# Optimization experiments

Hardware: AMD Instinct MI355X
Metric: run time of the kernel (lower is better)

Reference implementation:

```python
import jax, jax.numpy as jnp
import numpy as np

N_PIECES = 4
N_ACTIONS = 4
H = W = 4


def _conv3x3(x, w, b):
    # x: [B,C,H,W], w: [O,C,3,3] (torch OIHW), padding=1
    y = jax.lax.conv_general_dilated(x, w, window_strides=(1, 1), padding=((1, 1), (1, 1)),
                                     dimension_numbers=('NCHW', 'OIHW', 'NCHW'))
    return y + b[None, :, None, None]


def _conv1x1(x, w, b):
    # 1x1 conv as einsum; w: [O,C,1,1]
    return jnp.einsum('bchw,oc->bohw', x, w[:, :, 0, 0]) + b[None, :, None, None]


def setup_inputs() -> dict:
    key = jax.random.key(0)
    ks = jax.random.split(key, 20)
    B = 131072
    ob = jax.random.randint(ks[0], (B, H, W), 0, N_PIECES)
    ac = jax.random.randint(ks[1], (B,), 0, N_ACTIONS)

    def rnd(k, shape, fan_in):
        bound = 1.0 / np.sqrt(fan_in)
        return jax.random.uniform(k, shape, jnp.float32, -bound, bound)

    p = {}
    p['w_start1'] = rnd(ks[2], (32, N_PIECES + N_ACTIONS, 3, 3), 8 * 9)
    p['b_start1'] = rnd(ks[3], (32,), 8 * 9)
    p['w_start2'] = rnd(ks[4], (16, 32, 1, 1), 32)
    p['b_start2'] = rnd(ks[5], (16,), 32)
    p['w_ob1'] = rnd(ks[6], (16, 16, 1, 1), 16)
    p['b_ob1'] = rnd(ks[7], (16,), 16)
    p['w_ob2'] = rnd(ks[8], (N_PIECES * 2, 16 + N_PIECES, 1, 1), 20)
    p['b_ob2'] = rnd(ks[9], (N_PIECES * 2,), 20)
    p['w_reward'] = rnd(ks[10], (8, 16, 1, 1), 16)
    p['b_reward'] = rnd(ks[11], (8,), 16)
    p['fc_reward_w'] = rnd(ks[12], (4, 8 * H * W), 8 * H * W)
    p['fc_reward_b'] = rnd(ks[13], (4,), 8 * H * W)
    p['w_go'] = rnd(ks[14], (8, 16, 1, 1), 16)
    p['b_go'] = rnd(ks[15], (8,), 16)
    p['fc_go_w'] = rnd(ks[16], (4, 8 * H * W), 8 * H * W)
    p['fc_go_b'] = rnd(ks[17], (4,), 8 * H * W)
    return {'ob': ob, 'ac': ac, **p}


def reference(ob, ac, w_start1, b_start1, w_start2, b_start2, w_ob1, b_ob1, w_ob2, b_ob2,
              w_reward, b_reward, fc_reward_w, fc_reward_b, w_go, b_go, fc_go_w, fc_go_b):
    B = ob.shape[0]
    # one-hot encode board and action
    ob_oh = (ob[:, None, :, :] == jnp.arange(N_PIECES)[None, :, None, None]).astype(jnp.float32)  # [B,4,4,4]
    ac_oh = (ac[:, None] == jnp.arange(N_ACTIONS)[None, :]).astype(jnp.float32)  # [B,4]
    ac_map = jnp.broadcast_to(ac_oh[:, :, None, None], (B, N_ACTIONS, H, W))
    x = jnp.concatenate([ob_oh, ac_map], axis=1)  # [B,8,4,4]

    x = jax.nn.relu(_conv3x3(x, w_start1, b_start1))
    x = jax.nn.relu(_conv1x1(x, w_start2, b_start2))  # [B,16,4,4]

    # next-ob head
    nol = jax.nn.relu(_conv1x1(x, w_ob1, b_ob1))
    nol = jnp.concatenate([nol, ob_oh], axis=1)  # [B,20,4,4]
    nol = _conv1x1(nol, w_ob2, b_ob2)  # [B,8,4,4]
    nol = jnp.transpose(nol, (0, 2, 3, 1))  # [B,4,4,8]
    next_ob_loc = nol[..., :N_PIECES]
    next_ob_scale = nol[..., N_PIECES:]

    # reward head
    r = jax.nn.relu(_conv1x1(x, w_reward, b_reward)).reshape(B, -1)
    r = r @ fc_reward_w.T + fc_reward_b
    reward_loc, reward_scale = r[:, :2], r[:, 2:]

    # game-over head
    g = jax.nn.relu(_conv1x1(x, w_go, b_go)).reshape(B, -1)
    g = g @ fc_go_w.T + fc_go_b
    go_loc, go_scale = g[:, :2], g[:, 2:]

    return (next_ob_loc, next_ob_scale, reward_loc, reward_scale, go_loc, go_scale)
```

## Files before the change

kernel.cpp:

```cpp
#include <hip/hip_runtime.h>
#include <hip/hip_bf16.h>

typedef unsigned short u16;
typedef unsigned int u32;
typedef unsigned long long u64;

typedef _Float16 vh8 __attribute__((ext_vector_type(8)));
typedef _Float16 hv2 __attribute__((ext_vector_type(2)));
typedef __attribute__((ext_vector_type(16))) float vf16;

#define A1_OFF   0
#define A2_OFF   1280
#define A3_OFF   2048
#define A4_OFF   2560
#define FH_OFF   3072
#define FB_OFF   4096
#define FLAG_OFF 4104
#define T_OFF    4160

__device__ __forceinline__ float bf2f(u16 h){ union{u32 u; float f;} v; v.u=((u32)h)<<16; return v.f; }
__device__ __forceinline__ u16 f2h(float f){ _Float16 h=(_Float16)f; return __builtin_bit_cast(u16,h); }
__device__ __forceinline__ float ldw(const void* p,int i,bool bf){ return bf? bf2f(((const u16*)p)[i]) : ((const float*)p)[i]; }

__device__ __forceinline__ bool detect_bf16(const void* w1){
  const u16* p=(const u16*)w1; bool ok=true;
  for(int k=0;k<64;++k){ float v=bf2f(p[k]); ok &= (fabsf(v)<=0.125f); }
  return ok;
}

__device__ __constant__ int PI[32] = {0,1,2,3,8,9,10,11,4,5,6,7,12,13,14,15,
                                      16,17,18,19,24,25,26,27,20,21,22,23,28,29,30,31};

__global__ __launch_bounds__(256) void dw_prep(
    const void* w1, const void* b1, const void* w2, const void* b2,
    const void* wo1, const void* bo1, const void* wo2, const void* bo2,
    const void* wr, const void* br, const void* fcr, const void* fbr,
    const void* wg, const void* bg, const void* fcg, const void* fbg,
    u32* wsu){
  const int tid = threadIdx.x;
  const bool bf = detect_bf16(w1);
  float* wsf = (float*)wsu;

  for (int t=tid; t<768; t+=256){
    int kb=t>>8, l=(t>>2)&63, r=t&3, hi=l>>5, row=l&31;
    u32 w=0;
    for (int u=0;u<2;++u){
      int m=2*r+u, tt=m>>2, q=m&3, s=2*kb+tt;
      int pos = 2*s+hi;
      float v=0.f;
      if (s<5 && pos<=8) v = ldw(w1, row*72 + q*9 + pos, bf);
      w |= ((u32)f2h(v)) << (16*u);
    }
    wsu[A1_OFF+t]=w;
  }
  for (int t=tid; t<2048; t+=256){
    int a=t>>9, hi=(t>>8)&1, rq=(t>>6)&3, c16=(t>>2)&15, rl=t&3;
    int row = rl + 8*rq + 4*hi;
    int ci=c16>>2, cj=c16&3;
    float s0 = ldw(b1, row, bf);
    for (int dy=0; dy<3; ++dy)
      for (int dx=0; dx<3; ++dx){
        int ni=ci+dy-1, nj=cj+dx-1;
        if (ni>=0&&ni<4&&nj>=0&&nj<4)
          s0 += ldw(w1, row*72 + (4+a)*9 + dy*3+dx, bf);
      }
    wsf[T_OFF+t] = s0;
  }
  for (int t=tid; t<768; t+=256){
    int kb=t>>8, l=(t>>2)&63, r=t&3, hi=l>>5, row=l&31;
    int K0=kb*16+hi*8+2*r; u32 w=0;
    for (int s=0;s<2;++s){
      int K=K0+s; float v=0.f;
      if (K<32){ if(row<16) v=ldw(w2, row*32+PI[K], bf); }
      else if (K==32 && row<16) v=ldw(b2, row, bf);
      w |= ((u32)f2h(v)) << (16*s);
    }
    wsu[A2_OFF+t]=w;
  }
  for (int t=tid; t<512; t+=256){
    int kb=t>>8, l=(t>>2)&63, r=t&3, hi=l>>5, row=l&31;
    int K0=kb*16+hi*8+2*r; u32 w=0;
    for (int s=0;s<2;++s){
      int K=K0+s; float v=0.f;
      if (K<16){
        int c=PI[K];
        v = (row<16)? ldw(wo1,row*16+c,bf) : (row<24)? ldw(wr,(row-16)*16+c,bf) : ldw(wg,(row-24)*16+c,bf);
      } else if (K==16){
        v = (row<16)? ldw(bo1,row,bf) : (row<24)? ldw(br,row-16,bf) : ldw(bg,row-24,bf);
      }
      w |= ((u32)f2h(v)) << (16*s);
    }
    wsu[A3_OFF+t]=w;
  }
  for (int t=tid; t<512; t+=256){
    int kb=t>>8, l=(t>>2)&63, r=t&3, hi=l>>5, row=l&31;
    int K0=kb*16+hi*8+2*r; u32 w=0;
    for (int s=0;s<2;++s){
      int K=K0+s; float v=0.f;
      if (row<8){
        if (K<16)              v=ldw(wo2, row*20+PI[K], bf);
        else if (K==16)        v=ldw(bo2, row, bf);
        else if (K>=17&&K<=20) v=ldw(wo2, row*20+16+(K-17), bf);
      }
      w |= ((u32)f2h(v)) << (16*s);
    }
    wsu[A4_OFF+t]=w;
  }
  for (int t=tid; t<512; t+=256){
    int head=t>>8, r=t&255, hi=r>>7, c16=(r>>3)&15, k=(r>>1)&3, j=r&1;
    const void* f = head ? fcg : fcr;
    float v0 = ldw(f, k*128+(4*hi+2*j)*16+c16, bf);
    float v1 = ldw(f, k*128+(4*hi+2*j+1)*16+c16, bf);
    wsu[FH_OFF+t] = (u32)f2h(v0) | ((u32)f2h(v1)<<16);
  }
  for (int t=tid; t<8; t+=256) wsf[FB_OFF+t] = ldw(t<4?fbr:fbg, t&3, bf);
  if (tid==0) wsu[FLAG_OFF] = bf ? 1u : 0u;
}

__host__ __device__ constexpr u32 nbpgen(int c, int hi){
  u32 v=0;
  for (int s=0;s<5;++s){
    int pos=2*s+hi; u32 f=32;
    if (pos<=8){
      int ni=c/4+pos/3-1, nj=c%4+pos%3-1;
      if (ni>=0&&ni<4&&nj>=0&&nj<4) f=(u32)((ni*4+nj)<<1);
    }
    v |= f << (6*s);
  }
  return v;
}
__device__ __constant__ u32 NBP[32] = {
  nbpgen(0,0),nbpgen(1,0),nbpgen(2,0),nbpgen(3,0),nbpgen(4,0),nbpgen(5,0),nbpgen(6,0),nbpgen(7,0),
  nbpgen(8,0),nbpgen(9,0),nbpgen(10,0),nbpgen(11,0),nbpgen(12,0),nbpgen(13,0),nbpgen(14,0),nbpgen(15,0),
  nbpgen(0,1),nbpgen(1,1),nbpgen(2,1),nbpgen(3,1),nbpgen(4,1),nbpgen(5,1),nbpgen(6,1),nbpgen(7,1),
  nbpgen(8,1),nbpgen(9,1),nbpgen(10,1),nbpgen(11,1),nbpgen(12,1),nbpgen(13,1),nbpgen(14,1),nbpgen(15,1)};

__device__ __forceinline__ vf16 mfma(int4 a, int4 b, vf16 c){
  union{int4 i; vh8 v;} ua, ub; ua.i=a; ub.i=b;
  return __builtin_amdgcn_mfma_f32_32x32x16_f16(ua.v, ub.v, c, 0, 0, 0);
}
__device__ __forceinline__ u32 pkh(float a, float b){
#if __has_builtin(__builtin_amdgcn_cvt_pkrtz)
  auto h = __builtin_amdgcn_cvt_pkrtz(a, b);
  return __builtin_bit_cast(u32, h);
#else
  return (u32)f2h(a) | ((u32)f2h(b)<<16);
#endif
}
__device__ __forceinline__ u32 pkmax0(u32 x){
  u32 d; asm("v_pk_max_f16 %0, %1, 0" : "=v"(d) : "v"(x)); return d;
}
__device__ __forceinline__ float dot2(u32 w, u32 x, float c){
#if __has_builtin(__builtin_amdgcn_fdot2)
  return __builtin_amdgcn_fdot2(__builtin_bit_cast(hv2,w), __builtin_bit_cast(hv2,x), c, false);
#else
  hv2 a=__builtin_bit_cast(hv2,w), b=__builtin_bit_cast(hv2,x);
  return c + (float)a[0]*(float)b[0] + (float)a[1]*(float)b[1];
#endif
}
__device__ __forceinline__ u32 pkbf(float a, float b){
  u16 lo=__builtin_bit_cast(u16,__float2bfloat16(a));
  u16 hi=__builtin_bit_cast(u16,__float2bfloat16(b));
  return (u32)lo | ((u32)hi<<16);
}
template<int CTRL> __device__ __forceinline__ float dppadd(float x){
  int y=__builtin_amdgcn_update_dpp(0,__builtin_bit_cast(int,x),CTRL,0xF,0xF,false);
  return x+__builtin_bit_cast(float,y);
}
template<int CTRL> __device__ __forceinline__ u32 dppor(u32 x){
  u32 y=(u32)__builtin_amdgcn_update_dpp(0,(int)x,CTRL,0xF,0xF,false);
  return x|y;
}
template<int CTRL> __device__ __forceinline__ float dppmov(float x){
  int y=__builtin_amdgcn_update_dpp(0,__builtin_bit_cast(int,x),CTRL,0xF,0xF,false);
  return __builtin_bit_cast(float,y);
}

__global__ __launch_bounds__(512) void dw_main(
    const int* __restrict__ ob, const int* __restrict__ ac,
    const u32* __restrict__ g, void* __restrict__ outp, int B){
  __shared__ int4 sW4[576];
  __shared__ float4 sT4[512];
  const int4* gA = (const int4*)g;
  const float4* gT = (const float4*)g;

  const int tid  = threadIdx.x;
  if (tid < 512) sW4[tid] = gA[320+tid];
  if (tid < 64)  sW4[512+tid] = gA[320+512+tid];
  sT4[tid] = gT[(T_OFF>>2)+tid];
  __syncthreads();

  const int lane = tid & 63;
  const int hi   = lane >> 5;
  const int col  = lane & 31;
  const int c16  = col & 15;
  const int elem = col >> 4;
  const int wid  = tid >> 6;
  const bool obf = g[FLAG_OFF] != 0u;
  const float* gS = (const float*)g;

  const u32 nbp = NBP[(hi<<4)|c16];
  const int4 bconst = make_int4(hi?0:0x3C00, 0, 0, 0);
  const vf16 zero = {0.f,0.f,0.f,0.f,0.f,0.f,0.f,0.f,0.f,0.f,0.f,0.f,0.f,0.f,0.f,0.f};
  const int xaddr = (lane^32)<<2;

  const int e = (int)(blockIdx.x<<4) + (wid<<1) + elem;
  const bool act = (e < B);
  const int eL = act ? e : 0;

  u32 pkv = ((u32)ob[(size_t)eL*16 + c16]) << (c16<<1);
  pkv = dppor<0x121>(pkv);
  pkv = dppor<0x122>(pkv);
  pkv = dppor<0x124>(pkv);
  pkv = dppor<0x128>(pkv);
  const int a = ac[eL];

  int4 breg[3];
#pragma unroll
  for (int kb=0;kb<3;++kb){
    u32 w[4];
#pragma unroll
    for (int t=0;t<2;++t){
      const int s = kb*2+t;
      u32 w0=0, w1=0;
      if (s < 5){
        u32 v = (nbp >> (6*s)) & 63u;
        u32 np = (pkv >> (v & 31u)) & 3u;
        u32 src = (v < 32u) ? 0x3C00u : 0u;
        u64 oh = (u64)src << (np << 4);
        w0=(u32)oh; w1=(u32)(oh>>32);
      }
      w[2*t]=w0; w[2*t+1]=w1;
    }
    breg[kb]=make_int4(w[0],w[1],w[2],w[3]);
  }

  vf16 acc;
#pragma unroll
  for (int rq=0;rq<4;++rq){
    float4 q = sT4[(a*8 + hi*4 + rq)*16 + c16];
    acc[4*rq+0]=q.x; acc[4*rq+1]=q.y; acc[4*rq+2]=q.z; acc[4*rq+3]=q.w;
  }
#pragma unroll
  for (int kb=0;kb<3;++kb) acc = mfma(gA[(A1_OFF>>2)+kb*64+lane], breg[kb], acc);

  u32 zh[8];
#pragma unroll
  for (int i=0;i<8;++i) zh[i]=pkmax0(pkh(acc[2*i], acc[2*i+1]));
  vf16 acc2 = mfma(sW4[lane], make_int4(zh[0],zh[1],zh[2],zh[3]), zero);
  acc2 = mfma(sW4[64+lane], make_int4(zh[4],zh[5],zh[6],zh[7]), acc2);
  acc2 = mfma(sW4[128+lane], bconst, acc2);

  u32 xh[4];
#pragma unroll
  for (int i=0;i<4;++i) xh[i]=pkmax0(pkh(acc2[2*i], acc2[2*i+1]));
  vf16 acc3 = mfma(sW4[192+lane], make_int4(xh[0],xh[1],xh[2],xh[3]), zero);
  acc3 = mfma(sW4[256+lane], bconst, acc3);

  u32 nh[4];
#pragma unroll
  for (int i=0;i<4;++i) nh[i]=pkmax0(pkh(acc3[2*i], acc3[2*i+1]));
  const int p = (int)((pkv >> (c16<<1)) & 3u);
  u64 t64 = 0x3C00ull << (p<<4);
  u32 t_lo=(u32)t64, t_hi=(u32)(t64>>32);
  u32 pb0 = 0x3C00u | (t_lo<<16);
  u32 pb1 = (t_lo>>16) | (t_hi<<16);
  u32 pb2 = t_hi>>16;
  int4 B4b = make_int4(hi?0u:pb0, hi?0u:pb1, hi?0u:pb2, 0u);
  vf16 acc4 = mfma(sW4[320+lane], make_int4(nh[0],nh[1],nh[2],nh[3]), zero);
  acc4 = mfma(sW4[384+lane], B4b, acc4);

  if (act){
    size_t bofs=(size_t)e*64 + c16*4;
    size_t off = hi ? ((size_t)B*64 + bofs) : bofs;
    if (obf){
      u16* o16=(u16*)outp;
      *(uint2*)(o16+off) = make_uint2(pkbf(acc4[0],acc4[1]), pkbf(acc4[2],acc4[3]));
    } else {
      float* of=(float*)outp;
      *(float4*)(of+off) = make_float4(acc4[0],acc4[1],acc4[2],acc4[3]);
    }
  }

  u32 ra01 = pkmax0(pkh(acc3[8],  acc3[9]));
  u32 ra23 = pkmax0(pkh(acc3[10], acc3[11]));
  u32 ga01 = pkmax0(pkh(acc3[12], acc3[13]));
  u32 ga23 = pkmax0(pkh(acc3[14], acc3[15]));
  int4 tr0 = sW4[448 + hi*32 + c16*2];
  int4 tr1 = sW4[448 + hi*32 + c16*2 + 1];
  int4 tg0 = sW4[448 + 64 + hi*32 + c16*2];
  int4 tg1 = sW4[448 + 64 + hi*32 + c16*2 + 1];
  float rk[4], gk[4];
  rk[0] = dot2((u32)tr0.x, ra01, dot2((u32)tr0.y, ra23, 0.f));
  rk[1] = dot2((u32)tr0.z, ra01, dot2((u32)tr0.w, ra23, 0.f));
  rk[2] = dot2((u32)tr1.x, ra01, dot2((u32)tr1.y, ra23, 0.f));
  rk[3] = dot2((u32)tr1.z, ra01, dot2((u32)tr1.w, ra23, 0.f));
  gk[0] = dot2((u32)tg0.x, ga01, dot2((u32)tg0.y, ga23, 0.f));
  gk[1] = dot2((u32)tg0.z, ga01, dot2((u32)tg0.w, ga23, 0.f));
  gk[2] = dot2((u32)tg1.x, ga01, dot2((u32)tg1.y, ga23, 0.f));
  gk[3] = dot2((u32)tg1.z, ga01, dot2((u32)tg1.w, ga23, 0.f));

  const bool b0 = (c16&1), b1 = ((c16>>1)&1);
  float pr, pg;
  {
#pragma unroll
    for (int k=0;k<4;++k){ rk[k]=dppadd<0xB1>(rk[k]); gk[k]=dppadd<0xB1>(gk[k]); }
    float rp = b0 ? rk[2] : rk[0], rq = b0 ? rk[3] : rk[1];
    float gp = b0 ? gk[2] : gk[0], gq = b0 ? gk[3] : gk[1];
    rp=dppadd<0x4E>(rp); rq=dppadd<0x4E>(rq);
    gp=dppadd<0x4E>(gp); gq=dppadd<0x4E>(gq);
    pr = b1 ? rq : rp;
    pg = b1 ? gq : gp;
    pr=dppadd<0x124>(pr); pr=dppadd<0x128>(pr);
    pg=dppadd<0x124>(pg); pg=dppadd<0x128>(pg);
    int yr=__builtin_amdgcn_ds_bpermute(xaddr,__builtin_bit_cast(int,pr));
    int yg=__builtin_amdgcn_ds_bpermute(xaddr,__builtin_bit_cast(int,pg));
    pr += __builtin_bit_cast(float,yr);
    pg += __builtin_bit_cast(float,yg);
  }
  float yr2 = dppmov<0x4E>(pr);
  float yg2 = dppmov<0x4E>(pg);
  if (act && hi==0 && c16<2){
    float fb0 = gS[FB_OFF + (c16<<1)];
    float fb1 = gS[FB_OFF + (c16<<1)+1];
    float fb2 = gS[FB_OFF + 4 + (c16<<1)];
    float fb3 = gS[FB_OFF + 4 + (c16<<1)+1];
    if (obf){
      u32* o32=(u32*)outp;
      o32[(size_t)B*64 + (size_t)c16*B + e]     = pkbf(pr+fb0, yr2+fb1);
      o32[(size_t)B*64 + (size_t)(2+c16)*B + e] = pkbf(pg+fb2, yg2+fb3);
    } else {
      float* of=(float*)outp;
      *(float2*)(of + (size_t)B*128 + (size_t)c16*2*B + (size_t)e*2)     = make_float2(pr+fb0, yr2+fb1);
      *(float2*)(of + (size_t)B*128 + (size_t)(2+c16)*2*B + (size_t)e*2) = make_float2(pg+fb2, yg2+fb3);
    }
  }
}

extern "C" void kernel_launch(void* const* d_in, const int* in_sizes, int n_in,
                              void* d_out, int out_size, void* d_ws, size_t ws_size,
                              hipStream_t stream) {
  const int* ob = (const int*)d_in[0];
  const int* ac = (const int*)d_in[1];
  u32* ws = (u32*)d_ws;
  const int B = in_sizes[1];

  hipLaunchKernelGGL(dw_prep, dim3(1), dim3(256), 0, stream,
                     d_in[2], d_in[3], d_in[4], d_in[5], d_in[6], d_in[7],
                     d_in[8], d_in[9], d_in[10], d_in[11], d_in[12], d_in[13],
                     d_in[14], d_in[15], d_in[16], d_in[17], ws);

  const int nb = (B + 15) / 16;
  hipLaunchKernelGGL(dw_main, dim3(nb), dim3(512), 0, stream, ob, ac, ws, d_out, B);
}
```

Baseline: 53.41 us.

## Fold conv biases into accumulator init and drop bias MFMAs

Bias terms that were applied through extra MFMAs against a constant-one B operand are now precomputed as float tables. These tables initialise the accumulators directly. The next-ob one-hot contribution is folded into a per-piece bias table, which removes the second MFMA of the last layer. The weight and bias loads are also issued before the barrier, and the first-layer A fragments are prefetched into registers. This reduces MFMA count and shared memory use, but adds LDS bias reads and more live registers.

```diff
diff --git a/kernel.cpp b/kernel.cpp
--- a/kernel.cpp
+++ b/kernel.cpp
@@ -17,6 +17,7 @@
 #define FB_OFF   4096
 #define FLAG_OFF 4104
 #define T_OFF    4160
+#define BT_OFF   6208
 
 __device__ __forceinline__ float bf2f(u16 h){ union{u32 u; float f;} v; v.u=((u32)h)<<16; return v.f; }
 __device__ __forceinline__ u16 f2h(float f){ _Float16 h=(_Float16)f; return __builtin_bit_cast(u16,h); }
@@ -72,7 +73,6 @@
     for (int s=0;s<2;++s){
       int K=K0+s; float v=0.f;
       if (K<32){ if(row<16) v=ldw(w2, row*32+PI[K], bf); }
-      else if (K==32 && row<16) v=ldw(b2, row, bf);
       w |= ((u32)f2h(v)) << (16*s);
     }
     wsu[A2_OFF+t]=w;
@@ -85,8 +85,6 @@
       if (K<16){
         int c=PI[K];
         v = (row<16)? ldw(wo1,row*16+c,bf) : (row<24)? ldw(wr,(row-16)*16+c,bf) : ldw(wg,(row-24)*16+c,bf);
-      } else if (K==16){
-        v = (row<16)? ldw(bo1,row,bf) : (row<24)? ldw(br,row-16,bf) : ldw(bg,row-24,bf);
       }
       w |= ((u32)f2h(v)) << (16*s);
     }
@@ -97,11 +95,7 @@
     int K0=kb*16+hi*8+2*r; u32 w=0;
     for (int s=0;s<2;++s){
       int K=K0+s; float v=0.f;
-      if (row<8){
-        if (K<16)              v=ldw(wo2, row*20+PI[K], bf);
-        else if (K==16)        v=ldw(bo2, row, bf);
-        else if (K>=17&&K<=20) v=ldw(wo2, row*20+16+(K-17), bf);
-      }
+      if (row<8 && K<16) v=ldw(wo2, row*20+PI[K], bf);
       w |= ((u32)f2h(v)) << (16*s);
     }
     wsu[A4_OFF+t]=w;
@@ -114,6 +108,19 @@
     wsu[FH_OFF+t] = (u32)f2h(v0) | ((u32)f2h(v1)<<16);
   }
   for (int t=tid; t<8; t+=256) wsf[FB_OFF+t] = ldw(t<4?fbr:fbg, t&3, bf);
+  for (int t=tid; t<16; t+=256){
+    int hi=t>>3, rq=(t>>2)&1, rl=t&3; int row=rl+8*rq+4*hi;
+    wsf[BT_OFF+t] = ldw(b2,row,bf);
+  }
+  for (int t=tid; t<32; t+=256){
+    int hi=t>>4, rq=(t>>2)&3, rl=t&3; int row=rl+8*rq+4*hi;
+    float v = (row<16)? ldw(bo1,row,bf) : (row<24)? ldw(br,row-16,bf) : ldw(bg,row-24,bf);
+    wsf[BT_OFF+16+t]=v;
+  }
+  for (int t=tid; t<32; t+=256){
+    int p=t>>3, hi=(t>>2)&1, rl=t&3; int row=rl+4*hi;
+    wsf[BT_OFF+48+t] = ldw(bo2,row,bf) + ldw(wo2,row*20+16+p,bf);
+  }
   if (tid==0) wsu[FLAG_OFF] = bf ? 1u : 0u;
 }
 
@@ -179,41 +186,51 @@
 __global__ __launch_bounds__(512) void dw_main(
     const int* __restrict__ ob, const int* __restrict__ ac,
     const u32* __restrict__ g, void* __restrict__ outp, int B){
-  __shared__ int4 sW4[576];
+  __shared__ int4 sW4[384];
+  __shared__ float4 sBT4[20];
   __shared__ float4 sT4[512];
   const int4* gA = (const int4*)g;
   const float4* gT = (const float4*)g;
 
   const int tid  = threadIdx.x;
-  if (tid < 512) sW4[tid] = gA[320+tid];
-  if (tid < 64)  sW4[512+tid] = gA[320+512+tid];
-  sT4[tid] = gT[(T_OFF>>2)+tid];
-  __syncthreads();
-
   const int lane = tid & 63;
   const int hi   = lane >> 5;
   const int col  = lane & 31;
   const int c16  = col & 15;
   const int elem = col >> 4;
   const int wid  = tid >> 6;
-  const bool obf = g[FLAG_OFF] != 0u;
-  const float* gS = (const float*)g;
-
-  const u32 nbp = NBP[(hi<<4)|c16];
-  const int4 bconst = make_int4(hi?0:0x3C00, 0, 0, 0);
-  const vf16 zero = {0.f,0.f,0.f,0.f,0.f,0.f,0.f,0.f,0.f,0.f,0.f,0.f,0.f,0.f,0.f,0.f};
-  const int xaddr = (lane^32)<<2;
-
   const int e = (int)(blockIdx.x<<4) + (wid<<1) + elem;
   const bool act = (e < B);
   const int eL = act ? e : 0;
 
-  u32 pkv = ((u32)ob[(size_t)eL*16 + c16]) << (c16<<1);
+  int4 w4 = make_int4(0,0,0,0); float4 bt4 = make_float4(0,0,0,0);
+  const int srcw = tid + (tid<128 ? 320 : tid<192 ? 384 : tid<256 ? 448 : 512);
+  if (tid < 384) w4 = gA[srcw];
+  float4 t4 = gT[(T_OFF>>2)+tid];
+  if (tid >= 384 && tid < 404) bt4 = gT[(BT_OFF>>2)+(tid-384)];
+
+  const u32 obc = (u32)ob[(size_t)eL*16 + c16];
+  const int a = ac[eL];
+  int4 A1f[3];
+#pragma unroll
+  for (int kb=0;kb<3;++kb) A1f[kb]=gA[(A1_OFF>>2)+kb*64+lane];
+
+  if (tid < 384) sW4[tid] = w4;
+  sT4[tid] = t4;
+  if (tid >= 384 && tid < 404) sBT4[tid-384] = bt4;
+  __syncthreads();
+
+  const bool obf = g[FLAG_OFF] != 0u;
+  const float* gS = (const float*)g;
+  const u32 nbp = NBP[(hi<<4)|c16];
+  const vf16 zero = {0.f,0.f,0.f,0.f,0.f,0.f,0.f,0.f,0.f,0.f,0.f,0.f,0.f,0.f,0.f,0.f};
+  const int xaddr = (lane^32)<<2;
+
+  u32 pkv = obc << (c16<<1);
   pkv = dppor<0x121>(pkv);
   pkv = dppor<0x122>(pkv);
   pkv = dppor<0x124>(pkv);
   pkv = dppor<0x128>(pkv);
-  const int a = ac[eL];
 
   int4 breg[3];
 #pragma unroll
@@ -242,33 +259,41 @@
     acc[4*rq+0]=q.x; acc[4*rq+1]=q.y; acc[4*rq+2]=q.z; acc[4*rq+3]=q.w;
   }
 #pragma unroll
-  for (int kb=0;kb<3;++kb) acc = mfma(gA[(A1_OFF>>2)+kb*64+lane], breg[kb], acc);
+  for (int kb=0;kb<3;++kb) acc = mfma(A1f[kb], breg[kb], acc);
 
   u32 zh[8];
 #pragma unroll
   for (int i=0;i<8;++i) zh[i]=pkmax0(pkh(acc[2*i], acc[2*i+1]));
-  vf16 acc2 = mfma(sW4[lane], make_int4(zh[0],zh[1],zh[2],zh[3]), zero);
+  vf16 acc2 = zero;
+  {
+    float4 q0 = sBT4[hi*2], q1 = sBT4[hi*2+1];
+    acc2[0]=q0.x; acc2[1]=q0.y; acc2[2]=q0.z; acc2[3]=q0.w;
+    acc2[4]=q1.x; acc2[5]=q1.y; acc2[6]=q1.z; acc2[7]=q1.w;
+  }
+  acc2 = mfma(sW4[lane], make_int4(zh[0],zh[1],zh[2],zh[3]), acc2);
   acc2 = mfma(sW4[64+lane], make_int4(zh[4],zh[5],zh[6],zh[7]), acc2);
-  acc2 = mfma(sW4[128+lane], bconst, acc2);
 
   u32 xh[4];
 #pragma unroll
   for (int i=0;i<4;++i) xh[i]=pkmax0(pkh(acc2[2*i], acc2[2*i+1]));
-  vf16 acc3 = mfma(sW4[192+lane], make_int4(xh[0],xh[1],xh[2],xh[3]), zero);
-  acc3 = mfma(sW4[256+lane], bconst, acc3);
+  vf16 acc3;
+#pragma unroll
+  for (int rq=0;rq<4;++rq){
+    float4 q = sBT4[4 + hi*4 + rq];
+    acc3[4*rq+0]=q.x; acc3[4*rq+1]=q.y; acc3[4*rq+2]=q.z; acc3[4*rq+3]=q.w;
+  }
+  acc3 = mfma(sW4[128+lane], make_int4(xh[0],xh[1],xh[2],xh[3]), acc3);
 
   u32 nh[4];
 #pragma unroll
   for (int i=0;i<4;++i) nh[i]=pkmax0(pkh(acc3[2*i], acc3[2*i+1]));
   const int p = (int)((pkv >> (c16<<1)) & 3u);
-  u64 t64 = 0x3C00ull << (p<<4);
-  u32 t_lo=(u32)t64, t_hi=(u32)(t64>>32);
-  u32 pb0 = 0x3C00u | (t_lo<<16);
-  u32 pb1 = (t_lo>>16) | (t_hi<<16);
-  u32 pb2 = t_hi>>16;
-  int4 B4b = make_int4(hi?0u:pb0, hi?0u:pb1, hi?0u:pb2, 0u);
-  vf16 acc4 = mfma(sW4[320+lane], make_int4(nh[0],nh[1],nh[2],nh[3]), zero);
-  acc4 = mfma(sW4[384+lane], B4b, acc4);
+  vf16 acc4 = zero;
+  {
+    float4 q = sBT4[12 + p*2 + hi];
+    acc4[0]=q.x; acc4[1]=q.y; acc4[2]=q.z; acc4[3]=q.w;
+  }
+  acc4 = mfma(sW4[192+lane], make_int4(nh[0],nh[1],nh[2],nh[3]), acc4);
 
   if (act){
     size_t bofs=(size_t)e*64 + c16*4;
@@ -286,10 +311,10 @@
   u32 ra23 = pkmax0(pkh(acc3[10], acc3[11]));
   u32 ga01 = pkmax0(pkh(acc3[12], acc3[13]));
   u32 ga23 = pkmax0(pkh(acc3[14], acc3[15]));
-  int4 tr0 = sW4[448 + hi*32 + c16*2];
-  int4 tr1 = sW4[448 + hi*32 + c16*2 + 1];
-  int4 tg0 = sW4[448 + 64 + hi*32 + c16*2];
-  int4 tg1 = sW4[448 + 64 + hi*32 + c16*2 + 1];
+  int4 tr0 = sW4[256 + hi*32 + c16*2];
+  int4 tr1 = sW4[256 + hi*32 + c16*2 + 1];
+  int4 tg0 = sW4[256 + 64 + hi*32 + c16*2];
+  int4 tg1 = sW4[256 + 64 + hi*32 + c16*2 + 1];
   float rk[4], gk[4];
   rk[0] = dot2((u32)tr0.x, ra01, dot2((u32)tr0.y, ra23, 0.f));
   rk[1] = dot2((u32)tr0.z, ra01, dot2((u32)tr0.w, ra23, 0.f));
```

After: 54.16 us. About the same (+1.4%).
